# Kernel tuning notes

Hardware: AMD Instinct MI355X
Metric: run time of the kernel (lower is better)

Reference implementation:

```python
import jax, jax.numpy as jnp
import numpy as np

EPS = 1e-12  # F.normalize eps


def _norm_adj(flow):
    # flow: (T, C, C). PyG gcn_norm with self-loops on the dense cosine-sim graph.
    T = flow.shape[0]
    x = flow.reshape(T, -1)                                  # (T, N)
    xn = x / jnp.clip(jnp.linalg.norm(x, axis=1, keepdims=True), EPS)
    A = xn.T @ xn                                            # (N, N) cosine sims
    N = A.shape[0]
    deg = A.sum(axis=0) + 1.0                                # +1 from added self-loop weight
    dinv = jnp.where(deg > 0, jax.lax.rsqrt(deg), 0.0)
    return (A + jnp.eye(N, dtype=A.dtype)) * dinv[:, None] * dinv[None, :]


def setup_inputs() -> dict:
    key = jax.random.key(0)
    ks = jax.random.split(key, 8)
    B, T, C, E = 8, 24, 64, 32
    H = 32
    O = 32
    return {
        "Flow": jax.random.normal(ks[0], (B, T, C, C), dtype=jnp.float32),
        "Edge": jax.random.normal(ks[1], (B, C, C, E), dtype=jnp.float32),
        "W0": jax.random.normal(ks[2], (E, H), dtype=jnp.float32) * 0.1,
        "b0": jax.random.normal(ks[3], (H,), dtype=jnp.float32) * 0.1,
        "W1": jax.random.normal(ks[4], (H, H), dtype=jnp.float32) * 0.1,
        "b1": jax.random.normal(ks[5], (H,), dtype=jnp.float32) * 0.1,
        "W2": jax.random.normal(ks[6], (H, O), dtype=jnp.float32) * 0.1,
        "b2": jax.random.normal(ks[7], (O,), dtype=jnp.float32) * 0.1,
    }


def reference(Flow, Edge, W0, b0, W1, b1, W2, b2):
    B, C, _, E = Edge.shape

    def per_batch(flow, edge):
        A = _norm_adj(flow)                                  # (N, N)
        x = edge.reshape(C * C, E)                           # (N, E)
        for W, b in ((W0, b0), (W1, b1), (W2, b2)):
            x = jax.nn.relu(A @ (x @ W) + b)
        return x.reshape(C, C, -1)

    return jax.vmap(per_batch)(Flow, Edge)                   # (B, C, C, out)
```

## Files before the change

kernel.cpp:

```cpp
#include <hip/hip_runtime.h>

#define BB 8
#define TT 24
#define NN 4096
#define HH 32
#define JT 64
#define UPB (TT*HH)
#define CTRS 16
#define NT 512

__global__ __launch_bounds__(NT) void k_phase1(const float* __restrict__ Flow,
                                               const float* __restrict__ Edge,
                                               const float* __restrict__ W0,
                                               float* __restrict__ rn,
                                               float* __restrict__ s,
                                               float* __restrict__ uz,
                                               float* __restrict__ z0raw) {
    const int blk = blockIdx.x;
    const int tid = threadIdx.x;

    if (blk < BB * TT) {
        const float4* x = (const float4*)(Flow + (size_t)blk * NN);
        float sq = 0.f, sm = 0.f;
#pragma unroll
        for (int i = 0; i < 2; ++i) {
            float4 v = x[tid + i * NT];
            sq += v.x * v.x + v.y * v.y + v.z * v.z + v.w * v.w;
            sm += v.x + v.y + v.z + v.w;
        }
#pragma unroll
        for (int off = 32; off > 0; off >>= 1) {
            sq += __shfl_down(sq, off);
            sm += __shfl_down(sm, off);
        }
        __shared__ float rss[8], rsm[8];
        int wave = tid >> 6, lane = tid & 63;
        if (lane == 0) { rss[wave] = sq; rsm[wave] = sm; }
        __syncthreads();
        if (tid == 0) {
            float tss = 0.f, tsm = 0.f;
#pragma unroll
            for (int w = 0; w < 8; ++w) { tss += rss[w]; tsm += rsm[w]; }
            float r = 1.0f / fmaxf(sqrtf(tss), 1e-12f);
            rn[blk] = r;
            s[blk] = tsm * r;
        }
        int gid = blk * NT + tid;
        if (gid < 3 * BB * TT * HH + BB * CTRS) uz[gid] = 0.f;
    } else {
        const int g = blk - BB * TT;
        const int b = g >> 6;
        const int j0 = (g & 63) * JT;

        __shared__ float xs[JT][33];
        __shared__ float Ws[32][32];
        for (int i = tid; i < 1024; i += NT) Ws[i >> 5][i & 31] = W0[i];
        {
            float4 v = ((const float4*)(Edge + ((size_t)b * NN + j0) * HH))[tid];
            int r0 = tid >> 3, c0 = (tid & 7) * 4;
            xs[r0][c0] = v.x; xs[r0][c0 + 1] = v.y; xs[r0][c0 + 2] = v.z; xs[r0][c0 + 3] = v.w;
        }
        __syncthreads();
        const int r = tid >> 3;
        const int h0 = (tid & 7) * 4;
        float zr[4];
#pragma unroll
        for (int hh = 0; hh < 4; ++hh) {
            float acc = 0.f;
#pragma unroll
            for (int e = 0; e < 32; ++e) acc += xs[r][e] * Ws[e][h0 + hh];
            zr[hh] = acc;
        }
        float* zb = z0raw + ((size_t)b * NN + j0 + r) * HH + h0;
        ((float4*)zb)[0] = make_float4(zr[0], zr[1], zr[2], zr[3]);
    }
}

__global__ __launch_bounds__(NT) void k_dinvU0(const float* __restrict__ Flow,
                                               const float* __restrict__ rn,
                                               const float* __restrict__ s,
                                               const float* __restrict__ z0raw,
                                               float* __restrict__ dinv,
                                               float* __restrict__ u0) {
    const int blk = blockIdx.x;
    const int b = blk >> 6;
    const int j0 = (blk & 63) * JT;
    const int tid = threadIdx.x;

    __shared__ float xns[TT][JT];
    __shared__ float zs[JT][33];
    __shared__ float sS[TT];

    if (tid < TT) sS[tid] = s[b * TT + tid];
    {
        float4 v = ((const float4*)(z0raw + ((size_t)b * NN + j0) * HH))[tid];
        int r0 = tid >> 3, c0 = (tid & 7) * 4;
        zs[r0][c0] = v.x; zs[r0][c0 + 1] = v.y; zs[r0][c0 + 2] = v.z; zs[r0][c0 + 3] = v.w;
    }
    if (tid < TT * (JT / 4)) {
        int t = tid >> 4, c0 = (tid & 15) * 4;
        float4 v = ((const float4*)(Flow + (size_t)b * TT * NN + (size_t)t * NN + j0))[tid & 15];
        float rt = rn[b * TT + t];
        xns[t][c0] = v.x * rt; xns[t][c0 + 1] = v.y * rt;
        xns[t][c0 + 2] = v.z * rt; xns[t][c0 + 3] = v.w * rt;
    }
    __syncthreads();

    const int r = tid >> 3;
    const int h0 = (tid & 7) * 4;
    float deg = 1.0f;
#pragma unroll
    for (int t = 0; t < TT; ++t) deg += xns[t][r] * sS[t];
    const float di = (deg > 0.f) ? rsqrtf(deg) : 0.f;
    if ((tid & 7) == 0) dinv[b * NN + j0 + r] = di;
#pragma unroll
    for (int hh = 0; hh < 4; ++hh) zs[r][h0 + hh] *= di;
    __syncthreads();

#pragma unroll
    for (int k = 0; k < 2; ++k) {
        int p = tid + k * NT;
        if (p < UPB) {
            int t = p >> 5, h = p & 31;
            float acc = 0.f;
#pragma unroll 8
            for (int rr = 0; rr < JT; ++rr) acc += xns[t][rr] * zs[rr][h];
            atomicAdd(&u0[b * UPB + t * HH + h], acc);
        }
    }
}

__global__ __launch_bounds__(NT) void k_BA(const float* __restrict__ zraw_in,
                                           const float* __restrict__ Flow,
                                           const float* __restrict__ rn,
                                           const float* __restrict__ u_in,
                                           const float* __restrict__ dinv,
                                           const float* __restrict__ bias,
                                           const float* __restrict__ W,
                                           float* __restrict__ zraw_out,
                                           float* __restrict__ u_out) {
    const int blk = blockIdx.x;
    const int b = blk >> 6;
    const int j0 = (blk & 63) * JT;
    const int tid = threadIdx.x;

    __shared__ float us[TT][32];
    __shared__ float xns[TT][JT];
    __shared__ float Ws[32][32];
    __shared__ float xs[JT][33];
    __shared__ float zs[JT][33];
    __shared__ float bs[32];

    if (tid < 32) bs[tid] = bias[tid];
    for (int i = tid; i < 1024; i += NT) Ws[i >> 5][i & 31] = W[i];
    if (tid < UPB / 4) {
        float4 v = ((const float4*)(u_in + b * UPB))[tid];
        int t = tid >> 3, c0 = (tid & 7) * 4;
        us[t][c0] = v.x; us[t][c0 + 1] = v.y; us[t][c0 + 2] = v.z; us[t][c0 + 3] = v.w;
    }
    {
        float4 v = ((const float4*)(zraw_in + ((size_t)b * NN + j0) * HH))[tid];
        int r0 = tid >> 3, c0 = (tid & 7) * 4;
        zs[r0][c0] = v.x; zs[r0][c0 + 1] = v.y; zs[r0][c0 + 2] = v.z; zs[r0][c0 + 3] = v.w;
    }
    if (tid < TT * (JT / 4)) {
        int t = tid >> 4, c0 = (tid & 15) * 4;
        float4 v = ((const float4*)(Flow + (size_t)b * TT * NN + (size_t)t * NN + j0))[tid & 15];
        float rt = rn[b * TT + t];
        xns[t][c0] = v.x * rt; xns[t][c0 + 1] = v.y * rt;
        xns[t][c0 + 2] = v.z * rt; xns[t][c0 + 3] = v.w * rt;
    }
    const int r = tid >> 3;
    const int h0 = (tid & 7) * 4;
    const float di = dinv[b * NN + j0 + r];
    __syncthreads();

    float zreg[4];
#pragma unroll
    for (int hh = 0; hh < 4; ++hh) zreg[hh] = di * zs[r][h0 + hh];
#pragma unroll
    for (int hh = 0; hh < 4; ++hh) {
        int h = h0 + hh;
        float acc = 0.f;
#pragma unroll
        for (int t = 0; t < TT; ++t) acc += xns[t][r] * us[t][h];
        xs[r][h] = fmaxf(di * (acc + zreg[hh]) + bs[h], 0.f);
    }
    float zr[4];
#pragma unroll
    for (int hh = 0; hh < 4; ++hh) {
        float acc = 0.f;
#pragma unroll
        for (int e = 0; e < 32; ++e) acc += xs[r][e] * Ws[e][h0 + hh];
        zr[hh] = acc;
        zs[r][h0 + hh] = di * zr[hh];
    }
    float* zb = zraw_out + ((size_t)b * NN + j0 + r) * HH + h0;
    ((float4*)zb)[0] = make_float4(zr[0], zr[1], zr[2], zr[3]);
    __syncthreads();

#pragma unroll
    for (int k = 0; k < 2; ++k) {
        int p = tid + k * NT;
        if (p < UPB) {
            int t = p >> 5, h = p & 31;
            float acc = 0.f;
#pragma unroll 8
            for (int rr = 0; rr < JT; ++rr) acc += xns[t][rr] * zs[rr][h];
            atomicAdd(&u_out[b * UPB + t * HH + h], acc);
        }
    }
}

__global__ __launch_bounds__(NT, 4) void k_BAfin(const float* __restrict__ zraw_in,
                                                 const float* __restrict__ Flow,
                                                 const float* __restrict__ rn,
                                                 const float* __restrict__ u_in,
                                                 const float* __restrict__ dinv,
                                                 const float* __restrict__ bias1,
                                                 const float* __restrict__ W2,
                                                 const float* __restrict__ bias2,
                                                 float* __restrict__ u2,
                                                 unsigned* __restrict__ ctr,
                                                 float* __restrict__ out) {
    const int blk = blockIdx.x;
    const int b = blk >> 6;
    const int j0 = (blk & 63) * JT;
    const int tid = threadIdx.x;

    __shared__ float us[TT][32];
    __shared__ float xns[TT][JT];
    __shared__ float Ws[32][32];
    __shared__ float xs[JT][33];
    __shared__ float zs[JT][33];
    __shared__ float b1s[32], b2s[32];

    if (tid < 32) { b1s[tid] = bias1[tid]; b2s[tid] = bias2[tid]; }
    for (int i = tid; i < 1024; i += NT) Ws[i >> 5][i & 31] = W2[i];
    if (tid < UPB / 4) {
        float4 v = ((const float4*)(u_in + b * UPB))[tid];
        int t = tid >> 3, c0 = (tid & 7) * 4;
        us[t][c0] = v.x; us[t][c0 + 1] = v.y; us[t][c0 + 2] = v.z; us[t][c0 + 3] = v.w;
    }
    {
        float4 v = ((const float4*)(zraw_in + ((size_t)b * NN + j0) * HH))[tid];
        int r0 = tid >> 3, c0 = (tid & 7) * 4;
        zs[r0][c0] = v.x; zs[r0][c0 + 1] = v.y; zs[r0][c0 + 2] = v.z; zs[r0][c0 + 3] = v.w;
    }
    if (tid < TT * (JT / 4)) {
        int t = tid >> 4, c0 = (tid & 15) * 4;
        float4 v = ((const float4*)(Flow + (size_t)b * TT * NN + (size_t)t * NN + j0))[tid & 15];
        float rt = rn[b * TT + t];
        xns[t][c0] = v.x * rt; xns[t][c0 + 1] = v.y * rt;
        xns[t][c0 + 2] = v.z * rt; xns[t][c0 + 3] = v.w * rt;
    }
    const int r = tid >> 3;
    const int h0 = (tid & 7) * 4;
    const float di = dinv[b * NN + j0 + r];
    __syncthreads();

    float zreg[4];
#pragma unroll
    for (int hh = 0; hh < 4; ++hh) zreg[hh] = di * zs[r][h0 + hh];
#pragma unroll
    for (int hh = 0; hh < 4; ++hh) {
        int h = h0 + hh;
        float acc = 0.f;
#pragma unroll
        for (int t = 0; t < TT; ++t) acc += xns[t][r] * us[t][h];
        xs[r][h] = fmaxf(di * (acc + zreg[hh]) + b1s[h], 0.f);
    }
#pragma unroll
    for (int hh = 0; hh < 4; ++hh) {
        float acc = 0.f;
#pragma unroll
        for (int e = 0; e < 32; ++e) acc += xs[r][e] * Ws[e][h0 + hh];
        zs[r][h0 + hh] = di * acc;
    }
    __syncthreads();

#pragma unroll
    for (int k = 0; k < 2; ++k) {
        int p = tid + k * NT;
        if (p < UPB) {
            int t = p >> 5, h = p & 31;
            float acc = 0.f;
#pragma unroll 8
            for (int rr = 0; rr < JT; ++rr) acc += xns[t][rr] * zs[rr][h];
            atomicAdd(&u2[b * UPB + t * HH + h], acc);
        }
    }

    __syncthreads();
    if (tid == 0) {
        unsigned* c = ctr + b * CTRS;
        __hip_atomic_fetch_add(c, 1u, __ATOMIC_RELAXED, __HIP_MEMORY_SCOPE_AGENT);
        int lim = 1 << 22;
        while (__hip_atomic_load(c, __ATOMIC_RELAXED, __HIP_MEMORY_SCOPE_AGENT) < 64u && --lim)
            __builtin_amdgcn_s_sleep(1);
    }
    __syncthreads();

#pragma unroll
    for (int k = 0; k < 2; ++k) {
        int p = tid + k * NT;
        if (p < UPB)
            us[p >> 5][p & 31] = __hip_atomic_load(&u2[b * UPB + p], __ATOMIC_RELAXED,
                                                   __HIP_MEMORY_SCOPE_AGENT);
    }
    __syncthreads();

    float o[4];
#pragma unroll
    for (int hh = 0; hh < 4; ++hh) {
        int h = h0 + hh;
        float acc = 0.f;
#pragma unroll
        for (int t = 0; t < TT; ++t) acc += xns[t][r] * us[t][h];
        o[hh] = fmaxf(di * (acc + zs[r][h]) + b2s[h], 0.f);
    }
    float* orow = out + ((size_t)b * NN + j0 + r) * HH + h0;
    ((float4*)orow)[0] = make_float4(o[0], o[1], o[2], o[3]);
}

extern "C" void kernel_launch(void* const* d_in, const int* in_sizes, int n_in,
                              void* d_out, int out_size, void* d_ws, size_t ws_size,
                              hipStream_t stream) {
    const float* Flow = (const float*)d_in[0];
    const float* Edge = (const float*)d_in[1];
    const float* W0 = (const float*)d_in[2];
    const float* b0 = (const float*)d_in[3];
    const float* W1 = (const float*)d_in[4];
    const float* b1 = (const float*)d_in[5];
    const float* W2 = (const float*)d_in[6];
    const float* b2 = (const float*)d_in[7];
    float* out = (float*)d_out;

    float* ws = (float*)d_ws;
    float* rn    = ws;
    float* s     = rn + BB * TT;
    float* dinv  = s + BB * TT;
    float* zA    = dinv + (size_t)BB * NN;
    float* zB    = zA + (size_t)BB * NN * HH;
    float* u     = zB + (size_t)BB * NN * HH;
    unsigned* ctr = (unsigned*)(u + 3 * BB * UPB);
    float* u0 = u, *u1 = u + BB * UPB, *u2 = u + 2 * BB * UPB;

    k_phase1<<<dim3(BB * TT + 512), NT, 0, stream>>>(Flow, Edge, W0, rn, s, u, zA);
    k_dinvU0<<<dim3(512), NT, 0, stream>>>(Flow, rn, s, zA, dinv, u0);
    k_BA<<<dim3(512), NT, 0, stream>>>(zA, Flow, rn, u0, dinv, b0, W1, zB, u1);
    k_BAfin<<<dim3(512), NT, 0, stream>>>(zB, Flow, rn, u1, dinv, b1, W2, b2,
                                          u2, ctr, out);
}
```

Before: 41.62 us.

## Fuse degree/U0 and first GCN layer kernels with per-batch grid barrier

Merges the dinv/u0 kernel and the first BA layer kernel into one launch. Blocks of the same batch sync through an atomic counter spin-wait (with a bounded spin limit) before reading the accumulated u0. This removes one kernel launch and avoids reloading z, Flow tiles and dinv. The risk is deadlock or stalls if all 64 blocks of a batch are not co-resident, and launch_bounds(NT,4) is added to help occupancy.

Result: slower. 44.83 us (+7.7%).

```diff
diff --git a/kernel.cpp b/kernel.cpp
--- a/kernel.cpp
+++ b/kernel.cpp
@@ -46,7 +46,7 @@
             s[blk] = tsm * r;
         }
         int gid = blk * NT + tid;
-        if (gid < 3 * BB * TT * HH + BB * CTRS) uz[gid] = 0.f;
+        if (gid < 3 * BB * TT * HH + 2 * BB * CTRS) uz[gid] = 0.f;
     } else {
         const int g = blk - BB * TT;
         const int b = g >> 6;
@@ -76,12 +76,17 @@
     }
 }
 
-__global__ __launch_bounds__(NT) void k_dinvU0(const float* __restrict__ Flow,
+__global__ __launch_bounds__(NT, 4) void k_dBA(const float* __restrict__ Flow,
                                                const float* __restrict__ rn,
                                                const float* __restrict__ s,
                                                const float* __restrict__ z0raw,
+                                               const float* __restrict__ bias0,
+                                               const float* __restrict__ W1,
                                                float* __restrict__ dinv,
-                                               float* __restrict__ u0) {
+                                               float* __restrict__ u0,
+                                               float* __restrict__ u1,
+                                               unsigned* __restrict__ ctr,
+                                               float* __restrict__ z1raw) {
     const int blk = blockIdx.x;
     const int b = blk >> 6;
     const int j0 = (blk & 63) * JT;
@@ -89,9 +94,15 @@
 
     __shared__ float xns[TT][JT];
     __shared__ float zs[JT][33];
+    __shared__ float xs[JT][33];
+    __shared__ float Ws[32][32];
+    __shared__ float us[TT][32];
     __shared__ float sS[TT];
+    __shared__ float bs[32];
 
     if (tid < TT) sS[tid] = s[b * TT + tid];
+    if (tid < 32) bs[tid] = bias0[tid];
+    for (int i = tid; i < 1024; i += NT) Ws[i >> 5][i & 31] = W1[i];
     {
         float4 v = ((const float4*)(z0raw + ((size_t)b * NN + j0) * HH))[tid];
         int r0 = tid >> 3, c0 = (tid & 7) * 4;
@@ -128,63 +139,33 @@
             atomicAdd(&u0[b * UPB + t * HH + h], acc);
         }
     }
-}
-
-__global__ __launch_bounds__(NT) void k_BA(const float* __restrict__ zraw_in,
-                                           const float* __restrict__ Flow,
-                                           const float* __restrict__ rn,
-                                           const float* __restrict__ u_in,
-                                           const float* __restrict__ dinv,
-                                           const float* __restrict__ bias,
-                                           const float* __restrict__ W,
-                                           float* __restrict__ zraw_out,
-                                           float* __restrict__ u_out) {
-    const int blk = blockIdx.x;
-    const int b = blk >> 6;
-    const int j0 = (blk & 63) * JT;
-    const int tid = threadIdx.x;
-
-    __shared__ float us[TT][32];
-    __shared__ float xns[TT][JT];
-    __shared__ float Ws[32][32];
-    __shared__ float xs[JT][33];
-    __shared__ float zs[JT][33];
-    __shared__ float bs[32];
-
-    if (tid < 32) bs[tid] = bias[tid];
-    for (int i = tid; i < 1024; i += NT) Ws[i >> 5][i & 31] = W[i];
-    if (tid < UPB / 4) {
-        float4 v = ((const float4*)(u_in + b * UPB))[tid];
-        int t = tid >> 3, c0 = (tid & 7) * 4;
-        us[t][c0] = v.x; us[t][c0 + 1] = v.y; us[t][c0 + 2] = v.z; us[t][c0 + 3] = v.w;
-    }
-    {
-        float4 v = ((const float4*)(zraw_in + ((size_t)b * NN + j0) * HH))[tid];
-        int r0 = tid >> 3, c0 = (tid & 7) * 4;
-        zs[r0][c0] = v.x; zs[r0][c0 + 1] = v.y; zs[r0][c0 + 2] = v.z; zs[r0][c0 + 3] = v.w;
-    }
-    if (tid < TT * (JT / 4)) {
-        int t = tid >> 4, c0 = (tid & 15) * 4;
-        float4 v = ((const float4*)(Flow + (size_t)b * TT * NN + (size_t)t * NN + j0))[tid & 15];
-        float rt = rn[b * TT + t];
-        xns[t][c0] = v.x * rt; xns[t][c0 + 1] = v.y * rt;
-        xns[t][c0 + 2] = v.z * rt; xns[t][c0 + 3] = v.w * rt;
-    }
-    const int r = tid >> 3;
-    const int h0 = (tid & 7) * 4;
-    const float di = dinv[b * NN + j0 + r];
-    __syncthreads();
-
-    float zreg[4];
-#pragma unroll
-    for (int hh = 0; hh < 4; ++hh) zreg[hh] = di * zs[r][h0 + hh];
+
+    __syncthreads();
+    if (tid == 0) {
+        unsigned* c = ctr + b * CTRS;
+        __hip_atomic_fetch_add(c, 1u, __ATOMIC_RELAXED, __HIP_MEMORY_SCOPE_AGENT);
+        int lim = 1 << 22;
+        while (__hip_atomic_load(c, __ATOMIC_RELAXED, __HIP_MEMORY_SCOPE_AGENT) < 64u && --lim)
+            __builtin_amdgcn_s_sleep(1);
+    }
+    __syncthreads();
+
+#pragma unroll
+    for (int k = 0; k < 2; ++k) {
+        int p = tid + k * NT;
+        if (p < UPB)
+            us[p >> 5][p & 31] = __hip_atomic_load(&u0[b * UPB + p], __ATOMIC_RELAXED,
+                                                   __HIP_MEMORY_SCOPE_AGENT);
+    }
+    __syncthreads();
+
 #pragma unroll
     for (int hh = 0; hh < 4; ++hh) {
         int h = h0 + hh;
         float acc = 0.f;
 #pragma unroll
         for (int t = 0; t < TT; ++t) acc += xns[t][r] * us[t][h];
-        xs[r][h] = fmaxf(di * (acc + zreg[hh]) + bs[h], 0.f);
+        xs[r][h] = fmaxf(di * (acc + zs[r][h]) + bs[h], 0.f);
     }
     float zr[4];
 #pragma unroll
@@ -195,7 +176,7 @@
         zr[hh] = acc;
         zs[r][h0 + hh] = di * zr[hh];
     }
-    float* zb = zraw_out + ((size_t)b * NN + j0 + r) * HH + h0;
+    float* zb = z1raw + ((size_t)b * NN + j0 + r) * HH + h0;
     ((float4*)zb)[0] = make_float4(zr[0], zr[1], zr[2], zr[3]);
     __syncthreads();
 
@@ -207,7 +188,7 @@
             float acc = 0.f;
 #pragma unroll 8
             for (int rr = 0; rr < JT; ++rr) acc += xns[t][rr] * zs[rr][h];
-            atomicAdd(&u_out[b * UPB + t * HH + h], acc);
+            atomicAdd(&u1[b * UPB + t * HH + h], acc);
         }
     }
 }
@@ -345,10 +326,11 @@
     float* u     = zB + (size_t)BB * NN * HH;
     unsigned* ctr = (unsigned*)(u + 3 * BB * UPB);
     float* u0 = u, *u1 = u + BB * UPB, *u2 = u + 2 * BB * UPB;
+    unsigned* ctr0 = ctr;
+    unsigned* ctr1 = ctr + BB * CTRS;
 
     k_phase1<<<dim3(BB * TT + 512), NT, 0, stream>>>(Flow, Edge, W0, rn, s, u, zA);
-    k_dinvU0<<<dim3(512), NT, 0, stream>>>(Flow, rn, s, zA, dinv, u0);
-    k_BA<<<dim3(512), NT, 0, stream>>>(zA, Flow, rn, u0, dinv, b0, W1, zB, u1);
+    k_dBA<<<dim3(512), NT, 0, stream>>>(Flow, rn, s, zA, b0, W1, dinv, u0, u1, ctr0, zB);
     k_BAfin<<<dim3(512), NT, 0, stream>>>(zB, Flow, rn, u1, dinv, b1, W2, b2,
-                                          u2, ctr, out);
+                                          u2, ctr1, out);
 }
```
